# Kernel tuning notes

Measured on AMD Instinct MI355X. Metric: run time of the kernel, lower is better.

The kernel has to match this reference:

```python
import jax, jax.numpy as jnp
import numpy as np

TOP_K = 2

def setup_inputs() -> dict:
    key = jax.random.key(0)
    k1, k2, k3 = jax.random.split(key, 3)
    B, D, E = 32768, 768, 8
    h = jax.random.normal(k1, (B, D), dtype=jnp.float32)
    gate_w = jax.random.normal(k2, (E, D), dtype=jnp.float32) * 0.02
    gate_b = jax.random.normal(k3, (E,), dtype=jnp.float32) * 0.02
    return {"h": h, "gate_w": gate_w, "gate_b": gate_b}

def reference(h, gate_w, gate_b):
    # logits: [B, n_experts] = h @ W^T + b
    logits = jnp.einsum('bd,ed->be', h, gate_w) + gate_b
    # top-k over experts (eval path: no jitter noise)
    top_vals, indices = jax.lax.top_k(logits, TOP_K)   # [B, top_k]
    weights = jax.nn.softmax(top_vals, axis=-1)        # [B, top_k]
    return indices, weights, logits
```

## Files before the change

kernel.cpp:

```cpp
#include <hip/hip_runtime.h>
#include <hip/hip_bf16.h>
#include <math.h>


constexpr int D  = 768;
constexpr int E  = 8;
constexpr int D4 = D / 4;
constexpr int BLOCK = 256;
constexpr int GRID  = 1024;

__device__ __forceinline__ float dot4acc(float4 a, float4 b, float acc) {
    acc = fmaf(a.x, b.x, acc);
    acc = fmaf(a.y, b.y, acc);
    acc = fmaf(a.z, b.z, acc);
    acc = fmaf(a.w, b.w, acc);
    return acc;
}

__device__ __forceinline__ float wave_reduce8(float a[8], int lane) {
    {
        const bool hi = lane & 1;
#pragma unroll
        for (int j = 0; j < 4; ++j) {
            float send = hi ? a[j] : a[j + 4];
            float recv = __shfl_xor(send, 1, 64);
            float keep = hi ? a[j + 4] : a[j];
            a[j] = keep + recv;
        }
    }
    {
        const bool hi = lane & 2;
#pragma unroll
        for (int j = 0; j < 2; ++j) {
            float send = hi ? a[j] : a[j + 2];
            float recv = __shfl_xor(send, 2, 64);
            float keep = hi ? a[j + 2] : a[j];
            a[j] = keep + recv;
        }
    }
    {
        const bool hi = lane & 4;
        float send = hi ? a[0] : a[1];
        float recv = __shfl_xor(send, 4, 64);
        float keep = hi ? a[1] : a[0];
        a[0] = keep + recv;
    }
    float v = a[0];
    v += __shfl_xor(v, 8, 64);
    v += __shfl_xor(v, 16, 64);
    v += __shfl_xor(v, 32, 64);
    return v;
}

__device__ __forceinline__ void finalize_row(
        float v , int lane, int obase,
        int e_lane, int row,
        float* __restrict__ out_idx, float* __restrict__ out_w,
        float* __restrict__ out_logits) {
    float l[8];
    l[0] = __shfl(v, obase | 0, 64);
    l[1] = __shfl(v, obase | 4, 64);
    l[2] = __shfl(v, obase | 2, 64);
    l[3] = __shfl(v, obase | 6, 64);
    l[4] = __shfl(v, obase | 1, 64);
    l[5] = __shfl(v, obase | 5, 64);
    l[6] = __shfl(v, obase | 3, 64);
    l[7] = __shfl(v, obase | 7, 64);

    float v0 = l[0]; int i0 = 0;
    float v1 = -INFINITY; int i1 = -1;
#pragma unroll
    for (int e = 1; e < 8; ++e) {
        float x = l[e];
        bool gt0 = x > v0;
        bool gt1 = x > v1;
        float nv1 = gt0 ? v0 : (gt1 ? x : v1);
        int   ni1 = gt0 ? i0 : (gt1 ? e : i1);
        v1 = nv1; i1 = ni1;
        v0 = gt0 ? x : v0;
        i0 = gt0 ? e : i0;
    }
    float t = expf(v1 - v0);
    float w0 = 1.0f / (1.0f + t);
    float w1 = t * w0;

    if (lane < 2) {
        out_idx[row * 2 + lane] = (float)(lane ? i1 : i0);
        out_w  [row * 2 + lane] = lane ? w1 : w0;
    }
    if (lane < 8) {
        out_logits[row * 8 + e_lane] = v;
    }
}

__global__ __launch_bounds__(BLOCK, 4)
void topic_router_kernel(const float* __restrict__ h,
                         const float* __restrict__ gate_w,
                         const float* __restrict__ gate_b,
                         float* __restrict__ out_idx,
                         float* __restrict__ out_w,
                         float* __restrict__ out_logits,
                         int B) {
    __shared__ float gate_s[E * D];

    const int tid = threadIdx.x;
    const float4* gw4 = (const float4*)gate_w;
    float4* gs4 = (float4*)gate_s;
#pragma unroll
    for (int i = tid; i < E * D4; i += BLOCK) gs4[i] = gw4[i];
    __syncthreads();

    const int lane  = tid & 63;
    const int wave  = tid >> 6;
    const int gwave = blockIdx.x * (BLOCK / 64) + wave;
    const int nwaves = gridDim.x * (BLOCK / 64);

    const int l3 = lane & 7;
    const int e_lane = ((l3 & 1) << 2) | (l3 & 2) | ((l3 >> 2) & 1);
    const float bias = gate_b[e_lane];
    const int obase = lane & 56;

    const float4* h4 = (const float4*)h;
    const int npairs = B >> 1;

    for (int p = gwave; p < npairs; p += nwaves) {
        const int r0 = p * 2;
        const float4* hp0 = h4 + (size_t)r0 * D4 + lane;
        const float4* hp1 = hp0 + D4;

        float4 hv0[3], hv1[3];
#pragma unroll
        for (int c = 0; c < 3; ++c) hv0[c] = hp0[c * 64];
#pragma unroll
        for (int c = 0; c < 3; ++c) hv1[c] = hp1[c * 64];

        float acc0[E], acc1[E];
#pragma unroll
        for (int e = 0; e < E; ++e) { acc0[e] = 0.0f; acc1[e] = 0.0f; }

#pragma unroll
        for (int c = 0; c < 3; ++c) {
#pragma unroll
            for (int e = 0; e < E; ++e) {
                float4 g = gs4[e * D4 + c * 64 + lane];
                acc0[e] = dot4acc(hv0[c], g, acc0[e]);
                acc1[e] = dot4acc(hv1[c], g, acc1[e]);
            }
        }

        float va = wave_reduce8(acc0, lane) + bias;
        float vb = wave_reduce8(acc1, lane) + bias;
        finalize_row(va, lane, obase, e_lane, r0,     out_idx, out_w, out_logits);
        finalize_row(vb, lane, obase, e_lane, r0 + 1, out_idx, out_w, out_logits);
    }
}

extern "C" void kernel_launch(void* const* d_in, const int* in_sizes, int n_in,
                              void* d_out, int out_size, void* d_ws, size_t ws_size,
                              hipStream_t stream) {
    const float* h      = (const float*)d_in[0];
    const float* gate_w = (const float*)d_in[1];
    const float* gate_b = (const float*)d_in[2];

    const int B = in_sizes[0] / D;

    float* out        = (float*)d_out;
    float* out_idx    = out;
    float* out_w      = out + (size_t)B * 2;
    float* out_logits = out + (size_t)B * 4;

    topic_router_kernel<<<dim3(GRID), dim3(BLOCK), 0, stream>>>(
        h, gate_w, gate_b, out_idx, out_w, out_logits, B);
}
```

Before: 170.0 us.

## Split router into logits GEMV and per-row top-k kernels with register prefetch

Splits the fused kernel in two. The first kernel computes logits, prefetching the next row pair's activations into registers while it computes the current pair, and writes both rows' logits in one coalesced 16-lane store; it runs on half as many blocks. The second kernel reads the logits back with one thread per row and does the top-2 plus softmax with vectorized float2 stores. This removes the shuffle-heavy per-row finalize from the bandwidth-bound main loop, at the cost of a second launch, an extra logits round trip through memory, and higher register pressure from the prefetch buffers.

```diff
diff --git a/kernel.cpp b/kernel.cpp
--- a/kernel.cpp
+++ b/kernel.cpp
@@ -6,8 +6,8 @@
 constexpr int D  = 768;
 constexpr int E  = 8;
 constexpr int D4 = D / 4;
-constexpr int BLOCK = 256;
-constexpr int GRID  = 1024;
+constexpr int BLOCK  = 256;
+constexpr int GRID_A = 512;
 
 __device__ __forceinline__ float dot4acc(float4 a, float4 b, float acc) {
     acc = fmaf(a.x, b.x, acc);
@@ -52,20 +52,93 @@
     return v;
 }
 
-__device__ __forceinline__ void finalize_row(
-        float v , int lane, int obase,
-        int e_lane, int row,
-        float* __restrict__ out_idx, float* __restrict__ out_w,
-        float* __restrict__ out_logits) {
-    float l[8];
-    l[0] = __shfl(v, obase | 0, 64);
-    l[1] = __shfl(v, obase | 4, 64);
-    l[2] = __shfl(v, obase | 2, 64);
-    l[3] = __shfl(v, obase | 6, 64);
-    l[4] = __shfl(v, obase | 1, 64);
-    l[5] = __shfl(v, obase | 5, 64);
-    l[6] = __shfl(v, obase | 3, 64);
-    l[7] = __shfl(v, obase | 7, 64);
+__device__ __forceinline__ void load_pair(float4 dst[6], const float4* __restrict__ h4,
+                                          int pair, int lane) {
+    const float4* hp = h4 + (size_t)pair * (2 * D4) + lane;
+#pragma unroll
+    for (int c = 0; c < 3; ++c) dst[c]     = hp[c * 64];
+#pragma unroll
+    for (int c = 0; c < 3; ++c) dst[3 + c] = hp[D4 + c * 64];
+}
+
+__global__ __launch_bounds__(BLOCK, 4)
+void router_logits_kernel(const float* __restrict__ h,
+                          const float* __restrict__ gate_w,
+                          const float* __restrict__ gate_b,
+                          float* __restrict__ out_logits,
+                          int B) {
+    __shared__ float gate_s[E * D];
+
+    const int tid = threadIdx.x;
+    const float4* gw4 = (const float4*)gate_w;
+    float4* gs4 = (float4*)gate_s;
+#pragma unroll
+    for (int i = tid; i < E * D4; i += BLOCK) gs4[i] = gw4[i];
+    __syncthreads();
+
+    const int lane   = tid & 63;
+    const int wave   = tid >> 6;
+    const int gwave  = blockIdx.x * (BLOCK / 64) + wave;
+    const int nwaves = gridDim.x * (BLOCK / 64);
+
+    const int l3 = lane & 7;
+    const int e_lane = ((l3 & 1) << 2) | (l3 & 2) | ((l3 >> 2) & 1);
+    const float bias = gate_b[e_lane];
+
+    const float4* h4 = (const float4*)h;
+    const int npairs = B >> 1;
+
+    int p = gwave;
+    if (p >= npairs) return;
+
+    float4 cv[6];
+    load_pair(cv, h4, p, lane);
+
+    while (true) {
+        const int pn = p + nwaves;
+        const bool more = (pn < npairs);
+
+        float4 nv[6];
+        if (more) load_pair(nv, h4, pn, lane);
+
+        float acc0[E], acc1[E];
+#pragma unroll
+        for (int e = 0; e < E; ++e) { acc0[e] = 0.0f; acc1[e] = 0.0f; }
+
+#pragma unroll
+        for (int c = 0; c < 3; ++c) {
+#pragma unroll
+            for (int e = 0; e < E; ++e) {
+                float4 g = gs4[e * D4 + c * 64 + lane];
+                acc0[e] = dot4acc(cv[c],     g, acc0[e]);
+                acc1[e] = dot4acc(cv[3 + c], g, acc1[e]);
+            }
+        }
+
+        float va = wave_reduce8(acc0, lane) + bias;
+        float vb = wave_reduce8(acc1, lane) + bias;
+
+        float v = (lane & 8) ? vb : va;
+        if (lane < 16) out_logits[(size_t)p * 16 + (lane & 8) + e_lane] = v;
+
+        if (!more) break;
+#pragma unroll
+        for (int i = 0; i < 6; ++i) cv[i] = nv[i];
+        p = pn;
+    }
+}
+
+__global__ __launch_bounds__(BLOCK)
+void router_topk_kernel(const float* __restrict__ logits,
+                        float* __restrict__ out_idx,
+                        float* __restrict__ out_w,
+                        int B) {
+    const int t = blockIdx.x * BLOCK + threadIdx.x;
+    if (t >= B) return;
+
+    const float4* lp = (const float4*)(logits + (size_t)t * 8);
+    float4 a = lp[0], b = lp[1];
+    float l[8] = {a.x, a.y, a.z, a.w, b.x, b.y, b.z, b.w};
 
     float v0 = l[0]; int i0 = 0;
     float v1 = -INFINITY; int i1 = -1;
@@ -80,79 +153,12 @@
         v0 = gt0 ? x : v0;
         i0 = gt0 ? e : i0;
     }
-    float t = expf(v1 - v0);
-    float w0 = 1.0f / (1.0f + t);
-    float w1 = t * w0;
+    float tt = expf(v1 - v0);
+    float w0 = 1.0f / (1.0f + tt);
+    float w1 = tt * w0;
 
-    if (lane < 2) {
-        out_idx[row * 2 + lane] = (float)(lane ? i1 : i0);
-        out_w  [row * 2 + lane] = lane ? w1 : w0;
-    }
-    if (lane < 8) {
-        out_logits[row * 8 + e_lane] = v;
-    }
-}
-
-__global__ __launch_bounds__(BLOCK, 4)
-void topic_router_kernel(const float* __restrict__ h,
-                         const float* __restrict__ gate_w,
-                         const float* __restrict__ gate_b,
-                         float* __restrict__ out_idx,
-                         float* __restrict__ out_w,
-                         float* __restrict__ out_logits,
-                         int B) {
-    __shared__ float gate_s[E * D];
-
-    const int tid = threadIdx.x;
-    const float4* gw4 = (const float4*)gate_w;
-    float4* gs4 = (float4*)gate_s;
-#pragma unroll
-    for (int i = tid; i < E * D4; i += BLOCK) gs4[i] = gw4[i];
-    __syncthreads();
-
-    const int lane  = tid & 63;
-    const int wave  = tid >> 6;
-    const int gwave = blockIdx.x * (BLOCK / 64) + wave;
-    const int nwaves = gridDim.x * (BLOCK / 64);
-
-    const int l3 = lane & 7;
-    const int e_lane = ((l3 & 1) << 2) | (l3 & 2) | ((l3 >> 2) & 1);
-    const float bias = gate_b[e_lane];
-    const int obase = lane & 56;
-
-    const float4* h4 = (const float4*)h;
-    const int npairs = B >> 1;
-
-    for (int p = gwave; p < npairs; p += nwaves) {
-        const int r0 = p * 2;
-        const float4* hp0 = h4 + (size_t)r0 * D4 + lane;
-        const float4* hp1 = hp0 + D4;
-
-        float4 hv0[3], hv1[3];
-#pragma unroll
-        for (int c = 0; c < 3; ++c) hv0[c] = hp0[c * 64];
-#pragma unroll
-        for (int c = 0; c < 3; ++c) hv1[c] = hp1[c * 64];
-
-        float acc0[E], acc1[E];
-#pragma unroll
-        for (int e = 0; e < E; ++e) { acc0[e] = 0.0f; acc1[e] = 0.0f; }
-
-#pragma unroll
-        for (int c = 0; c < 3; ++c) {
-#pragma unroll
-            for (int e = 0; e < E; ++e) {
-                float4 g = gs4[e * D4 + c * 64 + lane];
-                acc0[e] = dot4acc(hv0[c], g, acc0[e]);
-                acc1[e] = dot4acc(hv1[c], g, acc1[e]);
-            }
-        }
-
-        float va = wave_reduce8(acc0, lane) + bias;
-        float vb = wave_reduce8(acc1, lane) + bias;
-        finalize_row(va, lane, obase, e_lane, r0,     out_idx, out_w, out_logits);
-        finalize_row(vb, lane, obase, e_lane, r0 + 1, out_idx, out_w, out_logits);
-    }
+    ((float2*)out_idx)[t] = make_float2((float)i0, (float)i1);
+    ((float2*)out_w)[t]   = make_float2(w0, w1);
 }
 
 extern "C" void kernel_launch(void* const* d_in, const int* in_sizes, int n_in,
@@ -169,6 +175,9 @@
     float* out_w      = out + (size_t)B * 2;
     float* out_logits = out + (size_t)B * 4;
 
-    topic_router_kernel<<<dim3(GRID), dim3(BLOCK), 0, stream>>>(
-        h, gate_w, gate_b, out_idx, out_w, out_logits, B);
+    router_logits_kernel<<<dim3(GRID_A), dim3(BLOCK), 0, stream>>>(
+        h, gate_w, gate_b, out_logits, B);
+
+    router_topk_kernel<<<dim3((B + BLOCK - 1) / BLOCK), dim3(BLOCK), 0, stream>>>(
+        out_logits, out_idx, out_w, B);
 }
```

New measurement: 208.7 us. 22.8% more time.
